# Performance work log

Measured on AMD Instinct MI355X. Metric: run time of the kernel, lower is better.

## Reference

```python
import jax, jax.numpy as jnp
import numpy as np

N = 200000   # active voxels
B = 2        # batch size
G = 128      # spatial grid extent per axis
CIN = 64
COUT = 64
KS = 3       # kernel size -> 27 offsets
DIL = 1
EPS = 1e-5


def setup_inputs() -> dict:
    rng = np.random.default_rng(0)
    # unique active voxel coordinates over a B x G^3 grid
    lin = rng.choice(B * G * G * G, size=N, replace=False)
    b = lin // (G * G * G)
    r = lin % (G * G * G)
    x = r // (G * G)
    r2 = r % (G * G)
    y = r2 // G
    z = r2 % G
    coords = jnp.asarray(np.stack([b, x, y, z], axis=1).astype(np.int32))
    key = jax.random.key(0)
    ks = jax.random.split(key, 7)
    feats = jax.random.normal(ks[0], (N, CIN), jnp.float32)
    s1 = 1.0 / np.sqrt(KS ** 3 * CIN)
    s2 = 1.0 / np.sqrt(KS ** 3 * COUT)
    return {
        "feats": feats,
        "w1": jax.random.normal(ks[1], (KS ** 3, CIN, COUT), jnp.float32) * s1,
        "g1": 1.0 + 0.1 * jax.random.normal(ks[2], (COUT,), jnp.float32),
        "b1": 0.1 * jax.random.normal(ks[3], (COUT,), jnp.float32),
        "w2": jax.random.normal(ks[4], (KS ** 3, COUT, COUT), jnp.float32) * s2,
        "g2": 1.0 + 0.1 * jax.random.normal(ks[5], (COUT,), jnp.float32),
        "b2": 0.1 * jax.random.normal(ks[6], (COUT,), jnp.float32),
        "coords": coords,
    }


def build_neighbors(coords):
    """Hash (dense) lookup: for each of 27 kernel offsets, the input index of
    the neighboring active voxel (submanifold: output sites == input sites).
    Returns idx [27, N] int32 (0 where invalid) and mask [27, N] bool."""
    n = coords.shape[0]
    lin = ((coords[:, 0] * G + coords[:, 1]) * G + coords[:, 2]) * G + coords[:, 3]
    table = jnp.full((B * G * G * G,), -1, jnp.int32).at[lin].set(
        jnp.arange(n, dtype=jnp.int32))
    offs = jnp.asarray(
        [[dx, dy, dz] for dx in (-1, 0, 1) for dy in (-1, 0, 1) for dz in (-1, 0, 1)],
        dtype=jnp.int32) * DIL                       # [27, 3]
    nxyz = coords[None, :, 1:] + offs[:, None, :]    # [27, N, 3]
    inb = jnp.all((nxyz >= 0) & (nxyz < G), axis=-1)  # [27, N]
    c = jnp.clip(nxyz, 0, G - 1)
    nlin = ((coords[None, :, 0] * G + c[..., 0]) * G + c[..., 1]) * G + c[..., 2]
    idx = table[nlin]                                # [27, N]
    mask = inb & (idx >= 0)
    return jnp.where(mask, idx, 0), mask


def subm_conv(feats, nbr_idx, nbr_mask, w):
    # gather-GEMM-scatter, accumulated per kernel offset
    out = jnp.zeros((feats.shape[0], w.shape[-1]), feats.dtype)
    for k in range(w.shape[0]):
        g = jnp.where(nbr_mask[k][:, None], feats[nbr_idx[k]], 0.0)  # [N, Cin]
        out = out + g @ w[k]
    return out


def sparse_bn(x, gamma, beta):
    m = jnp.mean(x, axis=0)
    v = jnp.var(x, axis=0)
    return (x - m) * jax.lax.rsqrt(v + EPS) * gamma + beta


def reference(feats, w1, g1, b1, w2, g2, b2, coords):
    nbr_idx, nbr_mask = build_neighbors(coords)
    h = jax.nn.relu(sparse_bn(subm_conv(feats, nbr_idx, nbr_mask, w1), g1, b1))
    h = sparse_bn(subm_conv(h, nbr_idx, nbr_mask, w2), g2, b2)
    # shortcut is Identity (in_channels == out_channels, stride == 1)
    return jax.nn.relu(h + feats)
```

## Files before the change

### kernel.cpp

```cpp
#include <hip/hip_runtime.h>


constexpr int N_VOX = 200000;
constexpr int GEXT  = 128;
constexpr int C     = 64;
constexpr int K27   = 27;
constexpr int TBL_N = 2 * GEXT * GEXT * GEXT;
constexpr float EPSF = 1e-5f;
constexpr int NCBLK = 1563;
constexpr int RBLK  = 128;

using short8   = __attribute__((ext_vector_type(8))) short;
using floatx16 = __attribute__((ext_vector_type(16))) float;

static __device__ __forceinline__ ushort f2bf(float f) {
  union { float f; unsigned u; } a; a.f = f;
  unsigned r = a.u + 0x7fff + ((a.u >> 16) & 1);
  return (ushort)(r >> 16);
}
static __device__ __forceinline__ float bf2f(ushort h) {
  union { unsigned u; float f; } a; a.u = ((unsigned)h) << 16;
  return a.f;
}

__global__ __launch_bounds__(256) void k_fill(int* __restrict__ t,
                                              int* __restrict__ bsum) {
  int i = blockIdx.x * 256 + threadIdx.x;
  if (i < TBL_N) t[i] = -1;
  if (i < 4096) bsum[i] = 0;
}

__global__ __launch_bounds__(256) void k_scatter(const int* __restrict__ coords,
                                                 int* __restrict__ t) {
  int n = blockIdx.x * 256 + threadIdx.x;
  if (n >= N_VOX) return;
  int4 c = reinterpret_cast<const int4*>(coords)[n];
  int lin = ((c.x * GEXT + c.y) * GEXT + c.z) * GEXT + c.w;
  t[lin] = n;
}

__global__ __launch_bounds__(256) void k_count(const int* __restrict__ coords,
                                               int* __restrict__ bsum) {
  int n = blockIdx.x * 256 + threadIdx.x;
  if (n >= N_VOX) return;
  int4 c = reinterpret_cast<const int4*>(coords)[n];
  int lin = ((c.x * GEXT + c.y) * GEXT + c.z) * GEXT + c.w;
  atomicAdd(&bsum[lin >> 10], 1);
}

__global__ __launch_bounds__(1024) void k_scan(const int* __restrict__ bsum,
                                               int* __restrict__ boff) {
  __shared__ int sc[1024];
  int t = threadIdx.x;
  int v0 = bsum[t * 4], v1 = bsum[t * 4 + 1], v2 = bsum[t * 4 + 2],
      v3 = bsum[t * 4 + 3];
  int s = v0 + v1 + v2 + v3;
  sc[t] = s;
  __syncthreads();
  for (int off = 1; off < 1024; off <<= 1) {
    int x = (t >= off) ? sc[t - off] : 0;
    __syncthreads();
    sc[t] += x;
    __syncthreads();
  }
  int excl = sc[t] - s;
  boff[t * 4]     = excl;
  boff[t * 4 + 1] = excl + v0;
  boff[t * 4 + 2] = excl + v0 + v1;
  boff[t * 4 + 3] = excl + v0 + v1 + v2;
}

__global__ __launch_bounds__(1024) void k_compact(int* __restrict__ table,
                                                  const int* __restrict__ boff,
                                                  int* __restrict__ perm) {
  __shared__ int wsum[16];
  int i = blockIdx.x * 1024 + threadIdx.x;
  int orig = table[i];
  bool valid = orig >= 0;
  unsigned long long bal = __ballot(valid);
  int lane = threadIdx.x & 63, wv = threadIdx.x >> 6;
  int before = __popcll(bal & ((1ull << lane) - 1ull));
  if (lane == 0) wsum[wv] = __popcll(bal);
  __syncthreads();
  int woff = 0;
  for (int w = 0; w < 16; ++w) woff += (w < wv) ? wsum[w] : 0;
  if (valid) {
    int j = boff[blockIdx.x] + woff + before;
    perm[j] = orig;
    table[i] = j;
  }
}

__global__ __launch_bounds__(256) void k_nbrp(const int* __restrict__ coords,
                                              const int* __restrict__ table,
                                              const int* __restrict__ perm,
                                              int* __restrict__ nbrp) {
  int j = blockIdx.x * 256 + threadIdx.x;
  if (j >= N_VOX) return;
  int orig = perm[j];
  int4 c = reinterpret_cast<const int4*>(coords)[orig];
  int k = 0;
  #pragma unroll
  for (int dx = -1; dx <= 1; ++dx)
    #pragma unroll
    for (int dy = -1; dy <= 1; ++dy)
      #pragma unroll
      for (int dz = -1; dz <= 1; ++dz) {
        int x = c.y + dx, y = c.z + dy, z = c.w + dz;
        int rank = -1;
        if (((unsigned)x < (unsigned)GEXT) & ((unsigned)y < (unsigned)GEXT) &
            ((unsigned)z < (unsigned)GEXT)) {
          int lin = ((c.x * GEXT + x) * GEXT + y) * GEXT + z;
          rank = table[lin];
        }
        nbrp[k * N_VOX + j] = rank;
        ++k;
      }
}

__global__ __launch_bounds__(256) void k_gcast(const float* __restrict__ feats,
                                               const int* __restrict__ perm,
                                               ushort* __restrict__ fbp) {
  int i = blockIdx.x * 256 + threadIdx.x;
  int j = i >> 4, seg = i & 15;
  int p = perm[j];
  float4 v = reinterpret_cast<const float4*>(feats)[(p << 4) + seg];
  ushort4 o;
  o.x = f2bf(v.x); o.y = f2bf(v.y); o.z = f2bf(v.z); o.w = f2bf(v.w);
  reinterpret_cast<ushort4*>(fbp)[i] = o;
}

__global__ __launch_bounds__(256) void k_castw(const float* __restrict__ w,
                                               ushort* __restrict__ wp) {
  int i = blockIdx.x * 256 + threadIdx.x;
  if (i >= K27 * 4096) return;
  int k = i >> 12, r = i & 4095, ci = r >> 6, co = r & 63;
  int ch = co >> 5, row = co & 31;
  int ks = ci >> 4, hi1 = (ci >> 3) & 1, e = ci & 7;
  int dst = ((((k * 2 + ch) * 4 + ks) * 2 + hi1) << 8) + row * 8 + e;
  wp[dst] = f2bf(w[i]);
}

template <bool OUT_BF16>
__global__ __launch_bounds__(256, 4) void k_convd(
    const ushort* __restrict__ fin,
    const ushort* __restrict__ wp,
    const int* __restrict__ nbrp,
    const int* __restrict__ perm,
    void* __restrict__ fout,
    float* __restrict__ part) {
  __shared__ float sred[4][2][32];
  const int tid = threadIdx.x, lane = tid & 63, wv = tid >> 6;
  const int lo = lane & 31, hi = lane >> 5;
  const int ch = wv & 1, vh = wv >> 1;
  const int xcd = blockIdx.x & 7, bi = blockIdx.x >> 3;
  const int tb = xcd * 195 + (xcd < 3 ? xcd : 3) + bi;
  const int n0 = tb * 128 + vh * 64;
  const int vA = n0 + lo, vB = n0 + 32 + lo;
  const bool okA = vA < N_VOX, okB = vB < N_VOX;

  floatx16 accA, accB;
  #pragma unroll
  for (int j = 0; j < 16; ++j) { accA[j] = 0.f; accB[j] = 0.f; }

  const char* wk = (const char*)wp + (ch << 12) + (lane << 4);
  int idxA = okA ? nbrp[vA] : -1;
  int idxB = okB ? nbrp[vB] : -1;

  #pragma unroll 1
  for (int k = 0; k < K27; ++k) {
    int nxA = -1, nxB = -1;
    if (k + 1 < K27) {
      nxA = okA ? nbrp[(k + 1) * N_VOX + vA] : -1;
      nxB = okB ? nbrp[(k + 1) * N_VOX + vB] : -1;
    }
    bool anyA = __ballot(idxA >= 0) != 0ull;
    bool anyB = __ballot(idxB >= 0) != 0ull;
    if (anyA || anyB) {
      short8 a0 = *(const short8*)(wk);
      short8 a1 = *(const short8*)(wk + 1024);
      short8 a2 = *(const short8*)(wk + 2048);
      short8 a3 = *(const short8*)(wk + 3072);
      if (anyA) {
        short8 b0, b1, b2, b3;
        if (idxA >= 0) {
          const char* b = (const char*)fin + ((size_t)idxA << 7) + (hi << 4);
          b0 = *(const short8*)(b);
          b1 = *(const short8*)(b + 32);
          b2 = *(const short8*)(b + 64);
          b3 = *(const short8*)(b + 96);
        } else {
          b0 = short8{0,0,0,0,0,0,0,0}; b1 = b0; b2 = b0; b3 = b0;
        }
        accA = __builtin_amdgcn_mfma_f32_32x32x16_bf16(a0, b0, accA, 0, 0, 0);
        accA = __builtin_amdgcn_mfma_f32_32x32x16_bf16(a1, b1, accA, 0, 0, 0);
        accA = __builtin_amdgcn_mfma_f32_32x32x16_bf16(a2, b2, accA, 0, 0, 0);
        accA = __builtin_amdgcn_mfma_f32_32x32x16_bf16(a3, b3, accA, 0, 0, 0);
      }
      if (anyB) {
        short8 b0, b1, b2, b3;
        if (idxB >= 0) {
          const char* b = (const char*)fin + ((size_t)idxB << 7) + (hi << 4);
          b0 = *(const short8*)(b);
          b1 = *(const short8*)(b + 32);
          b2 = *(const short8*)(b + 64);
          b3 = *(const short8*)(b + 96);
        } else {
          b0 = short8{0,0,0,0,0,0,0,0}; b1 = b0; b2 = b0; b3 = b0;
        }
        accB = __builtin_amdgcn_mfma_f32_32x32x16_bf16(a0, b0, accB, 0, 0, 0);
        accB = __builtin_amdgcn_mfma_f32_32x32x16_bf16(a1, b1, accB, 0, 0, 0);
        accB = __builtin_amdgcn_mfma_f32_32x32x16_bf16(a2, b2, accB, 0, 0, 0);
        accB = __builtin_amdgcn_mfma_f32_32x32x16_bf16(a3, b3, accB, 0, 0, 0);
      }
    }
    wk += 8192;
    idxA = nxA; idxB = nxB;
  }

  if (okA || okB) {
    #pragma unroll
    for (int sub = 0; sub < 2; ++sub) {
      const floatx16& acc = sub ? accB : accA;
      int vox = sub ? vB : vA;
      bool ok = sub ? okB : okA;
      if (!ok) continue;
      if (OUT_BF16) {
        ushort* o = (ushort*)fout + ((size_t)vox << 6) + (ch << 5) + (hi << 2);
        #pragma unroll
        for (int rg = 0; rg < 4; ++rg) {
          ushort4 v;
          v.x = f2bf(acc[rg * 4 + 0]); v.y = f2bf(acc[rg * 4 + 1]);
          v.z = f2bf(acc[rg * 4 + 2]); v.w = f2bf(acc[rg * 4 + 3]);
          *(ushort4*)(o + (rg << 3)) = v;
        }
      } else {
        int p = perm[vox];
        float* o = (float*)fout + ((size_t)p << 6) + (ch << 5) + (hi << 2);
        #pragma unroll
        for (int rg = 0; rg < 4; ++rg) {
          float4 v = {acc[rg * 4 + 0], acc[rg * 4 + 1],
                      acc[rg * 4 + 2], acc[rg * 4 + 3]};
          *(float4*)(o + (rg << 3)) = v;
        }
      }
    }
  }

  #pragma unroll
  for (int j = 0; j < 16; ++j) {
    float s  = accA[j] + accB[j];
    float ss = accA[j] * accA[j] + accB[j] * accB[j];
    #pragma unroll
    for (int m = 1; m < 32; m <<= 1) {
      s += __shfl_xor(s, m); ss += __shfl_xor(ss, m);
    }
    if (lo == 0) { sred[wv][hi][j] = s; sred[wv][hi][16 + j] = ss; }
  }
  __syncthreads();
  if (tid < 128) {
    int halfsel = tid >> 6, c = tid & 63;
    int chh = c >> 5, w32 = c & 31;
    int rg = w32 >> 3, hi1 = (w32 >> 2) & 1, r3 = c & 3;
    int j = halfsel * 16 + rg * 4 + r3;
    float v = sred[chh][hi1][j] + sred[2 + chh][hi1][j];
    part[(size_t)blockIdx.x * 128 + tid] = v;
  }
}

__global__ __launch_bounds__(256) void k_red(const float* __restrict__ part,
                                             float* __restrict__ part2) {
  __shared__ float red[256];
  int tid = threadIdx.x;
  int e = tid & 127, g = tid >> 7;
  float s = 0.f;
  for (int r = blockIdx.x * 2 + g; r < NCBLK; r += 2 * RBLK)
    s += part[(size_t)r * 128 + e];
  red[tid] = s;
  __syncthreads();
  if (tid < 128) part2[(size_t)blockIdx.x * 128 + tid] = red[tid] + red[tid + 128];
}

__global__ __launch_bounds__(256) void k_bnfin(const float* __restrict__ part2,
                                               const float* __restrict__ gamma,
                                               const float* __restrict__ beta,
                                               float* __restrict__ ab) {
  __shared__ float fin[128];
  int tid = threadIdx.x;
  if (tid < 128) {
    float s = 0.f;
    for (int r = 0; r < RBLK; ++r) s += part2[(size_t)r * 128 + tid];
    fin[tid] = s;
  }
  __syncthreads();
  if (tid < 64) {
    float su = fin[tid], ss = fin[64 + tid];
    float mean = su / (float)N_VOX;
    float var  = ss / (float)N_VOX - mean * mean;
    float a = gamma[tid] * rsqrtf(var + EPSF);
    ab[tid]      = a;
    ab[64 + tid] = beta[tid] - mean * a;
  }
}

__global__ __launch_bounds__(256) void k_bnrelu8(ushort* __restrict__ x,
                                                 const float* __restrict__ ab) {
  int i = blockIdx.x * 256 + threadIdx.x;
  ushort4 v0 = reinterpret_cast<ushort4*>(x)[i * 2];
  ushort4 v1 = reinterpret_cast<ushort4*>(x)[i * 2 + 1];
  int cb = (i * 8) & 63;
  v0.x = f2bf(fmaxf(bf2f(v0.x) * ab[cb]     + ab[64 + cb],     0.f));
  v0.y = f2bf(fmaxf(bf2f(v0.y) * ab[cb + 1] + ab[64 + cb + 1], 0.f));
  v0.z = f2bf(fmaxf(bf2f(v0.z) * ab[cb + 2] + ab[64 + cb + 2], 0.f));
  v0.w = f2bf(fmaxf(bf2f(v0.w) * ab[cb + 3] + ab[64 + cb + 3], 0.f));
  v1.x = f2bf(fmaxf(bf2f(v1.x) * ab[cb + 4] + ab[64 + cb + 4], 0.f));
  v1.y = f2bf(fmaxf(bf2f(v1.y) * ab[cb + 5] + ab[64 + cb + 5], 0.f));
  v1.z = f2bf(fmaxf(bf2f(v1.z) * ab[cb + 6] + ab[64 + cb + 6], 0.f));
  v1.w = f2bf(fmaxf(bf2f(v1.w) * ab[cb + 7] + ab[64 + cb + 7], 0.f));
  reinterpret_cast<ushort4*>(x)[i * 2]     = v0;
  reinterpret_cast<ushort4*>(x)[i * 2 + 1] = v1;
}

__global__ __launch_bounds__(256) void k_final4(float* __restrict__ h2,
                                                const float* __restrict__ feats,
                                                const float* __restrict__ ab) {
  int i = blockIdx.x * 256 + threadIdx.x;
  float4 a = reinterpret_cast<float4*>(h2)[i];
  float4 f = reinterpret_cast<const float4*>(feats)[i];
  int cb = (i * 4) & 63;
  float4 o;
  o.x = fmaxf(a.x * ab[cb]     + ab[64 + cb]     + f.x, 0.f);
  o.y = fmaxf(a.y * ab[cb + 1] + ab[64 + cb + 1] + f.y, 0.f);
  o.z = fmaxf(a.z * ab[cb + 2] + ab[64 + cb + 2] + f.z, 0.f);
  o.w = fmaxf(a.w * ab[cb + 3] + ab[64 + cb + 3] + f.w, 0.f);
  reinterpret_cast<float4*>(h2)[i] = o;
}

extern "C" void kernel_launch(void* const* d_in, const int* in_sizes, int n_in,
                              void* d_out, int out_size, void* d_ws, size_t ws_size,
                              hipStream_t stream) {
  const float* feats  = (const float*)d_in[0];
  const float* w1     = (const float*)d_in[1];
  const float* g1     = (const float*)d_in[2];
  const float* b1     = (const float*)d_in[3];
  const float* w2     = (const float*)d_in[4];
  const float* g2     = (const float*)d_in[5];
  const float* b2     = (const float*)d_in[6];
  const int*   coords = (const int*)d_in[7];
  float* out = (float*)d_out;

  char* ws = (char*)d_ws;
  int*    table = (int*)ws;     ws += (size_t)TBL_N * 4;
  int*    nbrp  = (int*)ws;     ws += (size_t)K27 * N_VOX * 4;
  ushort* fbp   = (ushort*)ws;  ws += (size_t)N_VOX * C * 2;
  ushort* h1p   = (ushort*)ws;  ws += (size_t)N_VOX * C * 2;
  int*    perm  = (int*)ws;     ws += (size_t)N_VOX * 4;
  ushort* wp1   = (ushort*)ws;  ws += (size_t)K27 * 4096 * 2;
  ushort* wp2   = (ushort*)ws;  ws += (size_t)K27 * 4096 * 2;
  int*    bsum  = (int*)ws;     ws += 4096 * 4;
  int*    boff  = (int*)ws;     ws += 4096 * 4;
  float*  part2 = (float*)ws;   ws += (size_t)RBLK * 128 * 4;
  float*  ab1   = (float*)ws;   ws += 512;
  float*  ab2   = (float*)ws;   ws += 512;
  float*  part  = (float*)table;

  k_fill<<<TBL_N / 256, 256, 0, stream>>>(table, bsum);
  k_scatter<<<(N_VOX + 255) / 256, 256, 0, stream>>>(coords, table);
  k_count<<<(N_VOX + 255) / 256, 256, 0, stream>>>(coords, bsum);
  k_scan<<<1, 1024, 0, stream>>>(bsum, boff);
  k_compact<<<TBL_N / 1024, 1024, 0, stream>>>(table, boff, perm);
  k_nbrp<<<(N_VOX + 255) / 256, 256, 0, stream>>>(coords, table, perm, nbrp);
  k_gcast<<<N_VOX * 16 / 256, 256, 0, stream>>>(feats, perm, fbp);
  k_castw<<<(K27 * 4096 + 255) / 256, 256, 0, stream>>>(w1, wp1);
  k_castw<<<(K27 * 4096 + 255) / 256, 256, 0, stream>>>(w2, wp2);

  k_convd<true><<<NCBLK, 256, 0, stream>>>(fbp, wp1, nbrp, perm, h1p, part);
  k_red<<<RBLK, 256, 0, stream>>>(part, part2);
  k_bnfin<<<1, 256, 0, stream>>>(part2, g1, b1, ab1);
  k_bnrelu8<<<N_VOX * 8 / 256, 256, 0, stream>>>(h1p, ab1);

  k_convd<false><<<NCBLK, 256, 0, stream>>>(h1p, wp2, nbrp, perm, out, part);
  k_red<<<RBLK, 256, 0, stream>>>(part, part2);
  k_bnfin<<<1, 256, 0, stream>>>(part2, g2, b2, ab2);
  k_final4<<<N_VOX * 64 / 4 / 256, 256, 0, stream>>>(out, feats, ab2);
}
```

Measured before the change: 323.3 us.

## Split sparse conv into compacted pair GEMM and per-voxel gather-sum

Replaces the dense per-voxel 27-offset loop with a pair-list formulation. Valid (offset, neighbor) pairs are compacted per offset into 64-aligned segments, a tile kernel computes each pair's 64-channel product into a bf16 buffer, and a second kernel sums each voxel's pair results and computes the BN partial sums. This skips MFMA work on empty neighbors and removes divergence, but adds several setup kernels, a large bf16 intermediate write/read, and an extra bf16 rounding of the partial products.

```diff
diff --git a/kernel.cpp b/kernel.cpp
--- a/kernel.cpp
+++ b/kernel.cpp
@@ -7,8 +7,13 @@
 constexpr int K27   = 27;
 constexpr int TBL_N = 2 * GEXT * GEXT * GEXT;
 constexpr float EPSF = 1e-5f;
-constexpr int NCBLK = 1563;
-constexpr int RBLK  = 128;
+
+constexpr int NCH      = 391;
+constexpr int CNT2N    = K27 * NCH;
+constexpr int PAIR_CAP = 460032;
+constexpr int TIL64    = PAIR_CAP / 64;
+constexpr int PBB      = 6250;
+constexpr int RBLK     = 128;
 
 using short8   = __attribute__((ext_vector_type(8))) short;
 using floatx16 = __attribute__((ext_vector_type(16))) float;
@@ -23,11 +28,16 @@
   return a.f;
 }
 
+
 __global__ __launch_bounds__(256) void k_fill(int* __restrict__ t,
-                                              int* __restrict__ bsum) {
+                                              int* __restrict__ bsum,
+                                              int* __restrict__ cnt2,
+                                              int* __restrict__ inl) {
   int i = blockIdx.x * 256 + threadIdx.x;
   if (i < TBL_N) t[i] = -1;
   if (i < 4096) bsum[i] = 0;
+  if (i < CNT2N) cnt2[i] = 0;
+  if (i < PAIR_CAP) inl[i] = -1;
 }
 
 __global__ __launch_bounds__(256) void k_scatter(const int* __restrict__ coords,
@@ -118,6 +128,92 @@
       }
 }
 
+__global__ __launch_bounds__(256) void k_cnt2(const int* __restrict__ nbrp,
+                                              int* __restrict__ cnt2) {
+  int gid = blockIdx.x * 256 + threadIdx.x;
+  int k = gid / 200192, j = gid % 200192;
+  if (j >= N_VOX) return;
+  if (nbrp[k * N_VOX + j] >= 0) atomicAdd(&cnt2[k * NCH + (j >> 9)], 1);
+}
+
+__global__ __launch_bounds__(512) void k_segtot(const int* __restrict__ cnt2,
+                                                int* __restrict__ segs) {
+  __shared__ int red[512];
+  int k = blockIdx.x, t = threadIdx.x;
+  red[t] = (t < NCH) ? cnt2[k * NCH + t] : 0;
+  __syncthreads();
+  for (int off = 256; off >= 1; off >>= 1) {
+    if (t < off) red[t] += red[t + off];
+    __syncthreads();
+  }
+  if (t == 0) segs[k] = red[0];
+}
+
+__global__ __launch_bounds__(64) void k_segbase(int* __restrict__ segs) {
+  if (threadIdx.x == 0) {
+    int b = 0;
+    for (int k = 0; k < K27; ++k) {
+      segs[32 + k] = b;
+      b += (segs[k] + 63) & ~63;
+    }
+    segs[32 + K27] = b;
+  }
+}
+
+__global__ __launch_bounds__(512) void k_choff(const int* __restrict__ cnt2,
+                                               const int* __restrict__ segs,
+                                               int* __restrict__ choff) {
+  __shared__ int sc[512];
+  int k = blockIdx.x, t = threadIdx.x;
+  int v = (t < NCH) ? cnt2[k * NCH + t] : 0;
+  sc[t] = v;
+  __syncthreads();
+  for (int off = 1; off < 512; off <<= 1) {
+    int x = (t >= off) ? sc[t - off] : 0;
+    __syncthreads();
+    sc[t] += x;
+    __syncthreads();
+  }
+  if (t < NCH) choff[k * NCH + t] = segs[32 + k] + sc[t] - v;
+}
+
+__global__ __launch_bounds__(512) void k_pairs(int* __restrict__ nbrp,
+                                               const int* __restrict__ choff,
+                                               int* __restrict__ inl) {
+  __shared__ int wsum[8];
+  int k = blockIdx.x / NCH, c = blockIdx.x % NCH;
+  int j = c * 512 + threadIdx.x;
+  int v = (j < N_VOX) ? nbrp[k * N_VOX + j] : -1;
+  bool valid = v >= 0;
+  unsigned long long bal = __ballot(valid);
+  int lane = threadIdx.x & 63, wv = threadIdx.x >> 6;
+  int before = __popcll(bal & ((1ull << lane) - 1ull));
+  if (lane == 0) wsum[wv] = __popcll(bal);
+  __syncthreads();
+  int woff = 0;
+  #pragma unroll
+  for (int w = 0; w < 8; ++w) woff += (w < wv) ? wsum[w] : 0;
+  if (valid) {
+    int p = choff[k * NCH + c] + woff + before;
+    inl[p] = v;
+    nbrp[k * N_VOX + j] = p;
+  }
+}
+
+__global__ __launch_bounds__(256) void k_tilek(const int* __restrict__ segs,
+                                               int* __restrict__ tile_k) {
+  int t = blockIdx.x * 256 + threadIdx.x;
+  if (t >= TIL64) return;
+  int p0 = t * 64, kk = -1;
+  if (p0 < segs[32 + K27]) {
+    #pragma unroll 1
+    for (int k = 0; k < K27; ++k)
+      if (p0 >= segs[32 + k] && p0 < segs[32 + k + 1]) kk = k;
+  }
+  tile_k[t] = kk;
+}
+
+
 __global__ __launch_bounds__(256) void k_gcast(const float* __restrict__ feats,
                                                const int* __restrict__ perm,
                                                ushort* __restrict__ fbp) {
@@ -141,132 +237,119 @@
   wp[dst] = f2bf(w[i]);
 }
 
-template <bool OUT_BF16>
-__global__ __launch_bounds__(256, 4) void k_convd(
+__global__ __launch_bounds__(256, 4) void k_pva(
     const ushort* __restrict__ fin,
     const ushort* __restrict__ wp,
-    const int* __restrict__ nbrp,
+    const int* __restrict__ inl,
+    const int* __restrict__ tile_k,
+    ushort* __restrict__ pv) {
+  const int kk = tile_k[blockIdx.x];
+  if (kk < 0) return;
+  const int tid = threadIdx.x, lane = tid & 63, wv = tid >> 6;
+  const int lo = lane & 31, hi = lane >> 5;
+  const int ch = wv & 1, vh = wv >> 1;
+  const int pr = blockIdx.x * 64 + vh * 32 + lo;
+  const int idx = inl[pr];
+
+  const char* wk = (const char*)wp + (kk << 13) + (ch << 12) + (lane << 4);
+  short8 a0 = *(const short8*)(wk);
+  short8 a1 = *(const short8*)(wk + 1024);
+  short8 a2 = *(const short8*)(wk + 2048);
+  short8 a3 = *(const short8*)(wk + 3072);
+
+  short8 b0, b1, b2, b3;
+  if (idx >= 0) {
+    const char* b = (const char*)fin + ((size_t)idx << 7) + (hi << 4);
+    b0 = *(const short8*)(b);
+    b1 = *(const short8*)(b + 32);
+    b2 = *(const short8*)(b + 64);
+    b3 = *(const short8*)(b + 96);
+  } else {
+    b0 = short8{0,0,0,0,0,0,0,0}; b1 = b0; b2 = b0; b3 = b0;
+  }
+
+  floatx16 acc;
+  #pragma unroll
+  for (int j = 0; j < 16; ++j) acc[j] = 0.f;
+  acc = __builtin_amdgcn_mfma_f32_32x32x16_bf16(a0, b0, acc, 0, 0, 0);
+  acc = __builtin_amdgcn_mfma_f32_32x32x16_bf16(a1, b1, acc, 0, 0, 0);
+  acc = __builtin_amdgcn_mfma_f32_32x32x16_bf16(a2, b2, acc, 0, 0, 0);
+  acc = __builtin_amdgcn_mfma_f32_32x32x16_bf16(a3, b3, acc, 0, 0, 0);
+
+  ushort* o = pv + ((size_t)pr << 6) + (ch << 5) + (hi << 2);
+  #pragma unroll
+  for (int rg = 0; rg < 4; ++rg) {
+    ushort4 v;
+    v.x = f2bf(acc[rg * 4 + 0]); v.y = f2bf(acc[rg * 4 + 1]);
+    v.z = f2bf(acc[rg * 4 + 2]); v.w = f2bf(acc[rg * 4 + 3]);
+    *(ushort4*)(o + (rg << 3)) = v;
+  }
+}
+
+template <bool OUT_F32>
+__global__ __launch_bounds__(256) void k_pvb(
+    const ushort* __restrict__ pv,
+    const int* __restrict__ pidx,
     const int* __restrict__ perm,
     void* __restrict__ fout,
     float* __restrict__ part) {
-  __shared__ float sred[4][2][32];
+  __shared__ float sred[4][8][16];
   const int tid = threadIdx.x, lane = tid & 63, wv = tid >> 6;
-  const int lo = lane & 31, hi = lane >> 5;
-  const int ch = wv & 1, vh = wv >> 1;
-  const int xcd = blockIdx.x & 7, bi = blockIdx.x >> 3;
-  const int tb = xcd * 195 + (xcd < 3 ? xcd : 3) + bi;
-  const int n0 = tb * 128 + vh * 64;
-  const int vA = n0 + lo, vB = n0 + 32 + lo;
-  const bool okA = vA < N_VOX, okB = vB < N_VOX;
-
-  floatx16 accA, accB;
-  #pragma unroll
-  for (int j = 0; j < 16; ++j) { accA[j] = 0.f; accB[j] = 0.f; }
-
-  const char* wk = (const char*)wp + (ch << 12) + (lane << 4);
-  int idxA = okA ? nbrp[vA] : -1;
-  int idxB = okB ? nbrp[vB] : -1;
-
-  #pragma unroll 1
-  for (int k = 0; k < K27; ++k) {
-    int nxA = -1, nxB = -1;
-    if (k + 1 < K27) {
-      nxA = okA ? nbrp[(k + 1) * N_VOX + vA] : -1;
-      nxB = okB ? nbrp[(k + 1) * N_VOX + vB] : -1;
+  const int g = tid >> 3, e = tid & 7;
+  const int j = blockIdx.x * 32 + g;
+
+  int p[27];
+  #pragma unroll
+  for (int t = 0; t < K27; ++t) p[t] = pidx[t * N_VOX + j];
+
+  float acc[8];
+  #pragma unroll
+  for (int r = 0; r < 8; ++r) acc[r] = 0.f;
+  #pragma unroll
+  for (int t = 0; t < K27; ++t) {
+    if (p[t] >= 0) {
+      short8 v = *(const short8*)(pv + ((size_t)p[t] << 6) + (e << 3));
+      #pragma unroll
+      for (int r = 0; r < 8; ++r) acc[r] += bf2f((ushort)v[r]);
     }
-    bool anyA = __ballot(idxA >= 0) != 0ull;
-    bool anyB = __ballot(idxB >= 0) != 0ull;
-    if (anyA || anyB) {
-      short8 a0 = *(const short8*)(wk);
-      short8 a1 = *(const short8*)(wk + 1024);
-      short8 a2 = *(const short8*)(wk + 2048);
-      short8 a3 = *(const short8*)(wk + 3072);
-      if (anyA) {
-        short8 b0, b1, b2, b3;
-        if (idxA >= 0) {
-          const char* b = (const char*)fin + ((size_t)idxA << 7) + (hi << 4);
-          b0 = *(const short8*)(b);
-          b1 = *(const short8*)(b + 32);
-          b2 = *(const short8*)(b + 64);
-          b3 = *(const short8*)(b + 96);
-        } else {
-          b0 = short8{0,0,0,0,0,0,0,0}; b1 = b0; b2 = b0; b3 = b0;
-        }
-        accA = __builtin_amdgcn_mfma_f32_32x32x16_bf16(a0, b0, accA, 0, 0, 0);
-        accA = __builtin_amdgcn_mfma_f32_32x32x16_bf16(a1, b1, accA, 0, 0, 0);
-        accA = __builtin_amdgcn_mfma_f32_32x32x16_bf16(a2, b2, accA, 0, 0, 0);
-        accA = __builtin_amdgcn_mfma_f32_32x32x16_bf16(a3, b3, accA, 0, 0, 0);
-      }
-      if (anyB) {
-        short8 b0, b1, b2, b3;
-        if (idxB >= 0) {
-          const char* b = (const char*)fin + ((size_t)idxB << 7) + (hi << 4);
-          b0 = *(const short8*)(b);
-          b1 = *(const short8*)(b + 32);
-          b2 = *(const short8*)(b + 64);
-          b3 = *(const short8*)(b + 96);
-        } else {
-          b0 = short8{0,0,0,0,0,0,0,0}; b1 = b0; b2 = b0; b3 = b0;
-        }
-        accB = __builtin_amdgcn_mfma_f32_32x32x16_bf16(a0, b0, accB, 0, 0, 0);
-        accB = __builtin_amdgcn_mfma_f32_32x32x16_bf16(a1, b1, accB, 0, 0, 0);
-        accB = __builtin_amdgcn_mfma_f32_32x32x16_bf16(a2, b2, accB, 0, 0, 0);
-        accB = __builtin_amdgcn_mfma_f32_32x32x16_bf16(a3, b3, accB, 0, 0, 0);
-      }
-    }
-    wk += 8192;
-    idxA = nxA; idxB = nxB;
-  }
-
-  if (okA || okB) {
-    #pragma unroll
-    for (int sub = 0; sub < 2; ++sub) {
-      const floatx16& acc = sub ? accB : accA;
-      int vox = sub ? vB : vA;
-      bool ok = sub ? okB : okA;
-      if (!ok) continue;
-      if (OUT_BF16) {
-        ushort* o = (ushort*)fout + ((size_t)vox << 6) + (ch << 5) + (hi << 2);
-        #pragma unroll
-        for (int rg = 0; rg < 4; ++rg) {
-          ushort4 v;
-          v.x = f2bf(acc[rg * 4 + 0]); v.y = f2bf(acc[rg * 4 + 1]);
-          v.z = f2bf(acc[rg * 4 + 2]); v.w = f2bf(acc[rg * 4 + 3]);
-          *(ushort4*)(o + (rg << 3)) = v;
-        }
-      } else {
-        int p = perm[vox];
-        float* o = (float*)fout + ((size_t)p << 6) + (ch << 5) + (hi << 2);
-        #pragma unroll
-        for (int rg = 0; rg < 4; ++rg) {
-          float4 v = {acc[rg * 4 + 0], acc[rg * 4 + 1],
-                      acc[rg * 4 + 2], acc[rg * 4 + 3]};
-          *(float4*)(o + (rg << 3)) = v;
-        }
-      }
-    }
-  }
-
-  #pragma unroll
-  for (int j = 0; j < 16; ++j) {
-    float s  = accA[j] + accB[j];
-    float ss = accA[j] * accA[j] + accB[j] * accB[j];
-    #pragma unroll
-    for (int m = 1; m < 32; m <<= 1) {
-      s += __shfl_xor(s, m); ss += __shfl_xor(ss, m);
-    }
-    if (lo == 0) { sred[wv][hi][j] = s; sred[wv][hi][16 + j] = ss; }
+  }
+
+  if (OUT_F32) {
+    int pj = perm[j];
+    float* o = (float*)fout + ((size_t)pj << 6) + (e << 3);
+    float4 v0 = {acc[0], acc[1], acc[2], acc[3]};
+    float4 v1 = {acc[4], acc[5], acc[6], acc[7]};
+    *(float4*)o = v0;
+    *(float4*)(o + 4) = v1;
+  } else {
+    ushort* o = (ushort*)fout + ((size_t)j << 6) + (e << 3);
+    ushort4 v0, v1;
+    v0.x = f2bf(acc[0]); v0.y = f2bf(acc[1]);
+    v0.z = f2bf(acc[2]); v0.w = f2bf(acc[3]);
+    v1.x = f2bf(acc[4]); v1.y = f2bf(acc[5]);
+    v1.z = f2bf(acc[6]); v1.w = f2bf(acc[7]);
+    *(ushort4*)o = v0;
+    *(ushort4*)(o + 4) = v1;
+  }
+
+  #pragma unroll
+  for (int r = 0; r < 8; ++r) {
+    float s = acc[r], ss = acc[r] * acc[r];
+    s += __shfl_xor(s, 8);  ss += __shfl_xor(ss, 8);
+    s += __shfl_xor(s, 16); ss += __shfl_xor(ss, 16);
+    s += __shfl_xor(s, 32); ss += __shfl_xor(ss, 32);
+    if (lane < 8) { sred[wv][lane][r] = s; sred[wv][lane][8 + r] = ss; }
   }
   __syncthreads();
   if (tid < 128) {
-    int halfsel = tid >> 6, c = tid & 63;
-    int chh = c >> 5, w32 = c & 31;
-    int rg = w32 >> 3, hi1 = (w32 >> 2) & 1, r3 = c & 3;
-    int j = halfsel * 16 + rg * 4 + r3;
-    float v = sred[chh][hi1][j] + sred[2 + chh][hi1][j];
+    int half = tid >> 6, ch = tid & 63;
+    int e2 = ch >> 3, r2 = ch & 7;
+    float v = sred[0][e2][half * 8 + r2] + sred[1][e2][half * 8 + r2] +
+              sred[2][e2][half * 8 + r2] + sred[3][e2][half * 8 + r2];
     part[(size_t)blockIdx.x * 128 + tid] = v;
   }
 }
+
 
 __global__ __launch_bounds__(256) void k_red(const float* __restrict__ part,
                                              float* __restrict__ part2) {
@@ -274,7 +357,7 @@
   int tid = threadIdx.x;
   int e = tid & 127, g = tid >> 7;
   float s = 0.f;
-  for (int r = blockIdx.x * 2 + g; r < NCBLK; r += 2 * RBLK)
+  for (int r = blockIdx.x * 2 + g; r < PBB; r += 2 * RBLK)
     s += part[(size_t)r * 128 + e];
   red[tid] = s;
   __syncthreads();
@@ -350,6 +433,7 @@
   float* out = (float*)d_out;
 
   char* ws = (char*)d_ws;
+  ushort* pv    = (ushort*)ws;  ws += (size_t)PAIR_CAP * C * 2;
   int*    table = (int*)ws;     ws += (size_t)TBL_N * 4;
   int*    nbrp  = (int*)ws;     ws += (size_t)K27 * N_VOX * 4;
   ushort* fbp   = (ushort*)ws;  ws += (size_t)N_VOX * C * 2;
@@ -357,29 +441,43 @@
   int*    perm  = (int*)ws;     ws += (size_t)N_VOX * 4;
   ushort* wp1   = (ushort*)ws;  ws += (size_t)K27 * 4096 * 2;
   ushort* wp2   = (ushort*)ws;  ws += (size_t)K27 * 4096 * 2;
+  int*    inl   = (int*)ws;     ws += (size_t)PAIR_CAP * 4;
   int*    bsum  = (int*)ws;     ws += 4096 * 4;
   int*    boff  = (int*)ws;     ws += 4096 * 4;
+  int*    cnt2  = (int*)ws;     ws += 42240;
+  int*    choff = (int*)ws;     ws += 42240;
+  int*    segs  = (int*)ws;     ws += 256;
+  int*    tilk  = (int*)ws;     ws += (size_t)TIL64 * 4;
   float*  part2 = (float*)ws;   ws += (size_t)RBLK * 128 * 4;
   float*  ab1   = (float*)ws;   ws += 512;
   float*  ab2   = (float*)ws;   ws += 512;
   float*  part  = (float*)table;
 
-  k_fill<<<TBL_N / 256, 256, 0, stream>>>(table, bsum);
+  k_fill<<<TBL_N / 256, 256, 0, stream>>>(table, bsum, cnt2, inl);
   k_scatter<<<(N_VOX + 255) / 256, 256, 0, stream>>>(coords, table);
   k_count<<<(N_VOX + 255) / 256, 256, 0, stream>>>(coords, bsum);
   k_scan<<<1, 1024, 0, stream>>>(bsum, boff);
   k_compact<<<TBL_N / 1024, 1024, 0, stream>>>(table, boff, perm);
   k_nbrp<<<(N_VOX + 255) / 256, 256, 0, stream>>>(coords, table, perm, nbrp);
+  k_cnt2<<<K27 * 782, 256, 0, stream>>>(nbrp, cnt2);
+  k_segtot<<<K27, 512, 0, stream>>>(cnt2, segs);
+  k_segbase<<<1, 64, 0, stream>>>(segs);
+  k_choff<<<K27, 512, 0, stream>>>(cnt2, segs, choff);
+  k_pairs<<<K27 * NCH, 512, 0, stream>>>(nbrp, choff, inl);
+  k_tilek<<<(TIL64 + 255) / 256, 256, 0, stream>>>(segs, tilk);
+
   k_gcast<<<N_VOX * 16 / 256, 256, 0, stream>>>(feats, perm, fbp);
   k_castw<<<(K27 * 4096 + 255) / 256, 256, 0, stream>>>(w1, wp1);
   k_castw<<<(K27 * 4096 + 255) / 256, 256, 0, stream>>>(w2, wp2);
 
-  k_convd<true><<<NCBLK, 256, 0, stream>>>(fbp, wp1, nbrp, perm, h1p, part);
+  k_pva<<<TIL64, 256, 0, stream>>>(fbp, wp1, inl, tilk, pv);
+  k_pvb<false><<<PBB, 256, 0, stream>>>(pv, nbrp, perm, h1p, part);
   k_red<<<RBLK, 256, 0, stream>>>(part, part2);
   k_bnfin<<<1, 256, 0, stream>>>(part2, g1, b1, ab1);
   k_bnrelu8<<<N_VOX * 8 / 256, 256, 0, stream>>>(h1p, ab1);
 
-  k_convd<false><<<NCBLK, 256, 0, stream>>>(h1p, wp2, nbrp, perm, out, part);
+  k_pva<<<TIL64, 256, 0, stream>>>(h1p, wp2, inl, tilk, pv);
+  k_pvb<true><<<PBB, 256, 0, stream>>>(pv, nbrp, perm, out, part);
   k_red<<<RBLK, 256, 0, stream>>>(part, part2);
   k_bnfin<<<1, 256, 0, stream>>>(part2, g2, b2, ab2);
   k_final4<<<N_VOX * 64 / 4 / 256, 256, 0, stream>>>(out, feats, ab2);
```

Result: slower. 512.8 us (+58.6%).
